# Kernel optimization log

Hardware: AMD Instinct MI355X
Metric: run time of the kernel (lower is better)

## Reference

```python
import jax, jax.numpy as jnp
import numpy as np

D_MODEL = 1024
N_HEADS = 16
HEAD_DIM = D_MODEL // N_HEADS
BATCH = 2
SEQ = 2048


def setup_inputs() -> dict:
    key = jax.random.key(0)
    ks = jax.random.split(key, 9)
    s = 1.0 / np.sqrt(D_MODEL)
    x = jax.random.normal(ks[0], (BATCH, SEQ, D_MODEL), dtype=jnp.float32)
    # causal mask, broadcastable to (B, H, S, S); positions with 0 are masked out
    mask = jnp.tril(jnp.ones((SEQ, SEQ), dtype=bool))[None, None, :, :]
    Wq = jax.random.normal(ks[1], (D_MODEL, D_MODEL), dtype=jnp.float32) * s
    Wk = jax.random.normal(ks[2], (D_MODEL, D_MODEL), dtype=jnp.float32) * s
    Wv = jax.random.normal(ks[3], (D_MODEL, D_MODEL), dtype=jnp.float32) * s
    Wo = jax.random.normal(ks[4], (D_MODEL, D_MODEL), dtype=jnp.float32) * s
    bq = jnp.zeros((D_MODEL,), jnp.float32)
    bk = jnp.zeros((D_MODEL,), jnp.float32)
    bv = jnp.zeros((D_MODEL,), jnp.float32)
    bo = jnp.zeros((D_MODEL,), jnp.float32)
    return {"x": x, "mask": mask, "Wq": Wq, "bq": bq, "Wk": Wk, "bk": bk,
            "Wv": Wv, "bv": bv, "Wo": Wo, "bo": bo}


def reference(x, mask, Wq, bq, Wk, bk, Wv, bv, Wo, bo):
    B, S, _ = x.shape
    scale = HEAD_DIM ** -0.5
    # nn.Linear: y = x @ W.T + b ; W stored as (out, in)
    def proj(W, b):
        y = jnp.einsum('bsd,ed->bse', x, W) + b
        return y.reshape(B, S, N_HEADS, HEAD_DIM).transpose(0, 2, 1, 3)  # (B,H,S,Dh)
    q = proj(Wq, bq)
    k = proj(Wk, bk)
    v = proj(Wv, bv)
    scores = jnp.einsum('bhqd,bhkd->bhqk', q, k) * scale  # (B,H,S,S)
    scores = jnp.where(mask, scores, jnp.float32(-jnp.inf))
    weights = jax.nn.softmax(scores, axis=-1)
    attn = jnp.einsum('bhqk,bhkd->bhqd', weights, v)
    attn = attn.transpose(0, 2, 1, 3).reshape(B, S, D_MODEL)
    out = jnp.einsum('bsd,ed->bse', attn, Wo) + bo
    return out
```

## Files before the change

kernel.cpp:

```cpp
#include <hip/hip_runtime.h>
#include <hip/hip_bf16.h>

using bf16x8 = __attribute__((ext_vector_type(8))) short;
using f32x4  = __attribute__((ext_vector_type(4))) float;

#define SEQ      2048
#define DMODEL   1024
#define NHEADS   16
#define HDIM     64
#define MROWS    4096

__device__ __forceinline__ unsigned short f2bf(float f) {
  union { float f; unsigned u; } c; c.f = f;
  unsigned r = c.u + 0x7FFFu + ((c.u >> 16) & 1u);
  return (unsigned short)(r >> 16);
}

__device__ __forceinline__ unsigned cvtpk(float a, float b) {
  unsigned r;
  asm("v_cvt_pk_bf16_f32 %0, %1, %2" : "=v"(r) : "v"(a), "v"(b));
  return r;
}

__device__ __forceinline__ void gload16(const void* g, void* s) {
  __builtin_amdgcn_global_load_lds(
      (const __attribute__((address_space(1))) void*)g,
      (__attribute__((address_space(3))) void*)s, 16, 0, 0);
}

__global__ void cvt_all(const float* __restrict__ x,  const float* __restrict__ wq,
                        const float* __restrict__ wk, const float* __restrict__ wv,
                        const float* __restrict__ wo,
                        unsigned short* __restrict__ xb,  unsigned short* __restrict__ wqb,
                        unsigned short* __restrict__ wkb, unsigned short* __restrict__ wvb,
                        unsigned short* __restrict__ wob)
{
  int i = blockIdx.x * blockDim.x + threadIdx.x;
  const float* src; unsigned short* dst; int off;
  if (i < 1048576) { src = x; dst = xb; off = i; }
  else {
    int k = i - 1048576, seg = k >> 18; off = k & 262143;
    if      (seg == 0) { src = wq; dst = wqb; }
    else if (seg == 1) { src = wk; dst = wkb; }
    else if (seg == 2) { src = wv; dst = wvb; }
    else               { src = wo; dst = wob; }
  }
  const float4 v = ((const float4*)src)[off];
  ushort4 o;
  o.x = f2bf(v.x); o.y = f2bf(v.y); o.z = f2bf(v.z); o.w = f2bf(v.w);
  ((ushort4*)dst)[off] = o;
}

__global__ __launch_bounds__(256, 4)
void gemm_qkv(const unsigned short* __restrict__ Ab,
              const unsigned short* __restrict__ Wqb,
              const unsigned short* __restrict__ Wkb,
              const unsigned short* __restrict__ Wvb,
              const float* __restrict__ bq, const float* __restrict__ bk,
              const float* __restrict__ bv,
              unsigned short* __restrict__ Qo, unsigned short* __restrict__ Ko,
              unsigned short* __restrict__ Vto)
{
  __shared__ unsigned short As[128 * 64];
  __shared__ unsigned short Bs[128 * 64];
  const int t  = threadIdx.x;
  const int w  = t >> 6, l = t & 63;
  const int lr = l & 15, lg = l >> 4;
  const int bm = blockIdx.x / 24;
  const int bn = blockIdx.x % 24;
  const int which = bn >> 3;
  const unsigned short* Bsrc = which == 0 ? Wqb : (which == 1 ? Wkb : Wvb);
  const float* biasp = which == 0 ? bq : (which == 1 ? bk : bv);
  const int bnw = bn & 7;
  const int wm = w >> 1, wn = w & 1;

  const char* Agp = (const char*)Ab + (size_t)bm * 128 * 2048;
  const char* Bgp = (const char*)Bsrc + (size_t)bnw * 128 * 2048;

  f32x4 acc[4][4];
  #pragma unroll
  for (int a = 0; a < 4; ++a)
    #pragma unroll
    for (int b = 0; b < 4; ++b) acc[a][b] = (f32x4){0.f, 0.f, 0.f, 0.f};

  for (int kt = 0; kt < 16; ++kt) {
    const int kbyte = kt * 128;
    #pragma unroll
    for (int i = 0; i < 4; ++i) {
      int idx  = i * 256 + t;
      int row  = idx >> 3;
      int colb = (idx & 7) << 4;
      gload16(Agp + (size_t)row * 2048 + kbyte + colb, (char*)As + idx * 16);
      gload16(Bgp + (size_t)row * 2048 + kbyte + colb, (char*)Bs + idx * 16);
    }
    __syncthreads();
    #pragma unroll
    for (int kk = 0; kk < 2; ++kk) {
      bf16x8 af[4], bfr[4];
      #pragma unroll
      for (int x = 0; x < 4; ++x) {
        af[x]  = *(const bf16x8*)&As[(wm * 64 + x * 16 + lr) * 64 + kk * 32 + lg * 8];
        bfr[x] = *(const bf16x8*)&Bs[(wn * 64 + x * 16 + lr) * 64 + kk * 32 + lg * 8];
      }
      #pragma unroll
      for (int xa = 0; xa < 4; ++xa)
        #pragma unroll
        for (int xb = 0; xb < 4; ++xb)
          acc[xa][xb] = __builtin_amdgcn_mfma_f32_16x16x32_bf16(af[xa], bfr[xb], acc[xa][xb], 0, 0, 0);
    }
    __syncthreads();
  }

  #pragma unroll
  for (int xb = 0; xb < 4; ++xb) {
    int colg = bnw * 128 + wn * 64 + xb * 16 + lr;
    int h  = colg >> 6, dh = colg & 63;
    float biasv = biasp[colg];
    #pragma unroll
    for (int xa = 0; xa < 4; ++xa) {
      int row0 = bm * 128 + wm * 64 + xa * 16 + lg * 4;
      #pragma unroll
      for (int i = 0; i < 4; ++i) {
        int m = row0 + i;
        int b = m >> 11, s = m & 2047;
        float v = acc[xa][xb][i] + biasv;
        if (which == 0) {
          Qo[(((size_t)(b * NHEADS + h)) * SEQ + s) * HDIM + dh] = f2bf(v * 0.180336881f);
        } else if (which == 1) {
          Ko[(((size_t)(b * NHEADS + h)) * SEQ + s) * HDIM + dh] = f2bf(v);
        } else {
          Vto[(((size_t)(b * NHEADS + h)) * HDIM + dh) * SEQ + s] = f2bf(v);
        }
      }
    }
  }
}

__device__ __forceinline__ void stage_kv64(const char* Kg, const char* Vg,
                                           char* Kl, char* Vl, int nb, int t)
{
  #pragma unroll
  for (int i = 0; i < 2; ++i) {
    int idx = i * 256 + t;
    int row = idx >> 3, colb = (idx & 7) << 4;
    int scol = colb ^ ((row & 7) << 4);
    gload16(Kg + (size_t)(nb + row) * 128 + scol, Kl + idx * 16);
    gload16(Vg + (size_t)row * 4096 + (size_t)nb * 2 + scol, Vl + idx * 16);
  }
}

__device__ __forceinline__ void attn_sub16(const char* Kl, const char* Vl, char* Pw,
                                           const bf16x8 (&qf)[2], const bf16x8 ones,
                                           f32x4 (&o)[4], f32x4 &accL,
                                           int q0w, int kbase, bool diag, int lr, int lg)
{
  bf16x8 kf[4][2];
  #pragma unroll
  for (int n = 0; n < 4; ++n)
    #pragma unroll
    for (int kk = 0; kk < 2; ++kk)
      kf[n][kk] = *(const bf16x8*)(Kl + (size_t)(n * 16 + lr) * 128 +
                                   ((kk * 64 + lg * 16) ^ ((lr & 7) << 4)));
  f32x4 st[4];
  __builtin_amdgcn_s_setprio(1);
  #pragma unroll
  for (int n = 0; n < 4; ++n) {
    f32x4 acc = (f32x4){0.f, 0.f, 0.f, 0.f};
    #pragma unroll
    for (int kk = 0; kk < 2; ++kk)
      acc = __builtin_amdgcn_mfma_f32_16x16x32_bf16(kf[n][kk], qf[kk], acc, 0, 0, 0);
    st[n] = acc;
  }
  __builtin_amdgcn_s_setprio(0);
  if (diag) {
    #pragma unroll
    for (int n = 0; n < 4; ++n) {
      #pragma unroll
      for (int i = 0; i < 4; ++i) {
        int key = kbase + n * 16 + lg * 4 + i;
        if (key > q0w + lr) st[n][i] = -3.0e38f;
      }
    }
  }
  #pragma unroll
  for (int n = 0; n < 4; ++n) {
    float p0 = exp2f(st[n][0]);
    float p1 = exp2f(st[n][1]);
    float p2 = exp2f(st[n][2]);
    float p3 = exp2f(st[n][3]);
    uint2 pw;
    pw.x = cvtpk(p0, p1);
    pw.y = cvtpk(p2, p3);
    *(uint2*)(Pw + lr * 128 + ((n * 32 + lg * 8) ^ ((lr & 7) << 4))) = pw;
  }
  __builtin_amdgcn_s_setprio(1);
  #pragma unroll
  for (int kk = 0; kk < 2; ++kk) {
    bf16x8 af = *(const bf16x8*)(Pw + lr * 128 + ((kk * 64 + lg * 16) ^ ((lr & 7) << 4)));
    accL = __builtin_amdgcn_mfma_f32_16x16x32_bf16(af, ones, accL, 0, 0, 0);
    #pragma unroll
    for (int n = 0; n < 4; ++n) {
      bf16x8 vf = *(const bf16x8*)(Vl + (size_t)(n * 16 + lr) * 128 +
                    ((kk * 64 + lg * 16) ^ ((lr & 7) << 4)));
      o[n] = __builtin_amdgcn_mfma_f32_16x16x32_bf16(af, vf, o[n], 0, 0, 0);
    }
  }
  __builtin_amdgcn_s_setprio(0);
}

__global__ __launch_bounds__(256, 4)
void attn_fwd(const unsigned short* __restrict__ Q,
              const unsigned short* __restrict__ K,
              const unsigned short* __restrict__ Vt,
              unsigned short* __restrict__ O)
{
  const int t = threadIdx.x;
  const int w = t >> 6, l = t & 63;
  const int lr = l & 15, lg = l >> 4;
  const int bh   = blockIdx.x & 31;
  const int slot = blockIdx.x >> 5;
  const int qt   = (slot < 8)  ? slot
                 : (slot < 16) ? (23 - slot)
                 : (slot < 24) ? slot
                 :               (55 - slot);
  const int b = bh >> 4, h = bh & 15;
  const int q0w = qt * 64 + w * 16;

  const unsigned short* Qp = Q + (size_t)bh * SEQ * HDIM;
  const char* Kg = (const char*)(K  + (size_t)bh * SEQ * HDIM);
  const char* Vg = (const char*)(Vt + (size_t)bh * HDIM * SEQ);

  __shared__ unsigned short Klds[2][64 * 64];
  __shared__ unsigned short Vlds[2][64 * 64];
  __shared__ unsigned short Plds[4][16][64];
  char* Pw = (char*)Plds[w];

  bf16x8 qf[2];
  #pragma unroll
  for (int kk = 0; kk < 2; ++kk)
    qf[kk] = *(const bf16x8*)(Qp + (size_t)(q0w + lr) * HDIM + kk * 32 + lg * 8);

  bf16x8 ones;
  #pragma unroll
  for (int e = 0; e < 8; ++e) ones[e] = (short)0x3F80;

  f32x4 o[4];
  f32x4 accL = (f32x4){0.f, 0.f, 0.f, 0.f};
  #pragma unroll
  for (int n = 0; n < 4; ++n) o[n] = (f32x4){0.f, 0.f, 0.f, 0.f};

  const int trips = qt + 1;

  stage_kv64(Kg, Vg, (char*)Klds[0], (char*)Vlds[0], 0, t);
  if (trips > 1)
    stage_kv64(Kg, Vg, (char*)Klds[1], (char*)Vlds[1], 64, t);

  int cur = 0;
  for (int kb = 0; kb < trips; ++kb) {
    if (kb + 1 < trips)
      asm volatile("s_waitcnt vmcnt(4)" ::: "memory");
    else
      asm volatile("s_waitcnt vmcnt(0)" ::: "memory");
    __builtin_amdgcn_s_barrier();
    asm volatile("" ::: "memory");
    attn_sub16((const char*)Klds[cur], (const char*)Vlds[cur], Pw, qf, ones,
               o, accL, q0w, kb * 64, kb == trips - 1, lr, lg);
    asm volatile("" ::: "memory");
    __builtin_amdgcn_s_barrier();
    asm volatile("" ::: "memory");
    if (kb + 2 < trips)
      stage_kv64(Kg, Vg, (char*)Klds[cur], (char*)Vlds[cur], (kb + 2) * 64, t);
    cur ^= 1;
  }

  #pragma unroll
  for (int n = 0; n < 4; ++n) {
    int col = h * HDIM + n * 16 + lr;
    #pragma unroll
    for (int i = 0; i < 4; ++i) {
      int srow = q0w + lg * 4 + i;
      O[((size_t)(b * SEQ + srow)) * DMODEL + col] = f2bf(o[n][i] / accL[i]);
    }
  }
}

__global__ __launch_bounds__(256, 2)
void gemm_out(const unsigned short* __restrict__ Ab, const unsigned short* __restrict__ Bb,
              const float* __restrict__ bias, float* __restrict__ C)
{
  __shared__ unsigned short As[128 * 64];
  __shared__ unsigned short Bs[64 * 64];
  const int t  = threadIdx.x;
  const int w  = t >> 6, l = t & 63;
  const int lr = l & 15, lg = l >> 4;
  const int bm = blockIdx.x >> 4;
  const int bn = blockIdx.x & 15;
  const int wm = w >> 1, wn = w & 1;

  const char* Agp = (const char*)Ab + (size_t)bm * 128 * 2048;
  const char* Bgp = (const char*)Bb + (size_t)bn * 64 * 2048;

  f32x4 acc[4][2];
  #pragma unroll
  for (int a = 0; a < 4; ++a)
    #pragma unroll
    for (int b = 0; b < 2; ++b) acc[a][b] = (f32x4){0.f, 0.f, 0.f, 0.f};

  for (int kt = 0; kt < 16; ++kt) {
    const int kbyte = kt * 128;
    #pragma unroll
    for (int i = 0; i < 4; ++i) {
      int idx  = i * 256 + t;
      int row  = idx >> 3;
      int colb = (idx & 7) << 4;
      gload16(Agp + (size_t)row * 2048 + kbyte + colb, (char*)As + idx * 16);
    }
    #pragma unroll
    for (int i = 0; i < 2; ++i) {
      int idx  = i * 256 + t;
      int row  = idx >> 3;
      int colb = (idx & 7) << 4;
      gload16(Bgp + (size_t)row * 2048 + kbyte + colb, (char*)Bs + idx * 16);
    }
    __syncthreads();
    #pragma unroll
    for (int kk = 0; kk < 2; ++kk) {
      bf16x8 af[4], bfr[2];
      #pragma unroll
      for (int x = 0; x < 4; ++x)
        af[x]  = *(const bf16x8*)&As[(wm * 64 + x * 16 + lr) * 64 + kk * 32 + lg * 8];
      #pragma unroll
      for (int x = 0; x < 2; ++x)
        bfr[x] = *(const bf16x8*)&Bs[(wn * 32 + x * 16 + lr) * 64 + kk * 32 + lg * 8];
      #pragma unroll
      for (int xa = 0; xa < 4; ++xa)
        #pragma unroll
        for (int xb = 0; xb < 2; ++xb)
          acc[xa][xb] = __builtin_amdgcn_mfma_f32_16x16x32_bf16(af[xa], bfr[xb], acc[xa][xb], 0, 0, 0);
    }
    __syncthreads();
  }
  #pragma unroll
  for (int xb = 0; xb < 2; ++xb) {
    int col = bn * 64 + wn * 32 + xb * 16 + lr;
    float bvv = bias[col];
    #pragma unroll
    for (int xa = 0; xa < 4; ++xa) {
      int row0 = bm * 128 + wm * 64 + xa * 16 + lg * 4;
      #pragma unroll
      for (int i = 0; i < 4; ++i)
        C[(size_t)(row0 + i) * DMODEL + col] = acc[xa][xb][i] + bvv;
    }
  }
}

extern "C" void kernel_launch(void* const* d_in, const int* in_sizes, int n_in,
                              void* d_out, int out_size, void* d_ws, size_t ws_size,
                              hipStream_t stream)
{
  const float* x  = (const float*)d_in[0];
  const float* Wq = (const float*)d_in[2];
  const float* bq = (const float*)d_in[3];
  const float* Wk = (const float*)d_in[4];
  const float* bk = (const float*)d_in[5];
  const float* Wv = (const float*)d_in[6];
  const float* bv = (const float*)d_in[7];
  const float* Wo = (const float*)d_in[8];
  const float* bo = (const float*)d_in[9];

  char* ws = (char*)d_ws;
  const size_t MB = 1024 * 1024;
  unsigned short* xb   = (unsigned short*)(ws + 0);
  unsigned short* Wqb  = (unsigned short*)(ws + 8  * MB);
  unsigned short* Wkb  = (unsigned short*)(ws + 10 * MB);
  unsigned short* Wvb  = (unsigned short*)(ws + 12 * MB);
  unsigned short* Wob  = (unsigned short*)(ws + 14 * MB);
  unsigned short* Qb   = (unsigned short*)(ws + 16 * MB);
  unsigned short* Kb   = (unsigned short*)(ws + 24 * MB);
  unsigned short* Vtb  = (unsigned short*)(ws + 32 * MB);
  unsigned short* Attn = (unsigned short*)(ws + 40 * MB);

  cvt_all<<<8192, 256, 0, stream>>>(x, Wq, Wk, Wv, Wo, xb, Wqb, Wkb, Wvb, Wob);
  gemm_qkv<<<768, 256, 0, stream>>>(xb, Wqb, Wkb, Wvb, bq, bk, bv, Qb, Kb, Vtb);
  attn_fwd<<<1024, 256, 0, stream>>>(Qb, Kb, Vtb, Attn);
  gemm_out<<<512, 256, 0, stream>>>(Attn, Wob, bo, (float*)d_out);
}
```

Baseline: 114.1 us.

## Pair causal q-tiles per block, swizzle GEMM LDS, use raw v_exp_f32

The attention kernel now gives each block two complementary query tiles (p and 31-p), so every block runs a uniform 33 KV iterations. This balances the causal triangle and halves the grid, with launch bounds lowered to 2 blocks per SU to make room for doubled accumulator registers. Both GEMMs gain an XOR swizzle on LDS columns to avoid bank conflicts on MFMA fragment reads. The softmax exp2f is replaced with raw v_exp_f32, which drops denormal and range handling. The costs are more registers per thread and lower occupancy in attention.

```diff
diff --git a/kernel.cpp b/kernel.cpp
--- a/kernel.cpp
+++ b/kernel.cpp
@@ -19,6 +19,12 @@
 __device__ __forceinline__ unsigned cvtpk(float a, float b) {
   unsigned r;
   asm("v_cvt_pk_bf16_f32 %0, %1, %2" : "=v"(r) : "v"(a), "v"(b));
+  return r;
+}
+
+__device__ __forceinline__ float fexp2(float x) {
+  float r;
+  asm("v_exp_f32 %0, %1" : "=v"(r) : "v"(x));
   return r;
 }
 
@@ -90,8 +96,9 @@
       int idx  = i * 256 + t;
       int row  = idx >> 3;
       int colb = (idx & 7) << 4;
-      gload16(Agp + (size_t)row * 2048 + kbyte + colb, (char*)As + idx * 16);
-      gload16(Bgp + (size_t)row * 2048 + kbyte + colb, (char*)Bs + idx * 16);
+      int scol = colb ^ ((row & 7) << 4);
+      gload16(Agp + (size_t)row * 2048 + kbyte + scol, (char*)As + idx * 16);
+      gload16(Bgp + (size_t)row * 2048 + kbyte + scol, (char*)Bs + idx * 16);
     }
     __syncthreads();
     #pragma unroll
@@ -99,8 +106,11 @@
       bf16x8 af[4], bfr[4];
       #pragma unroll
       for (int x = 0; x < 4; ++x) {
-        af[x]  = *(const bf16x8*)&As[(wm * 64 + x * 16 + lr) * 64 + kk * 32 + lg * 8];
-        bfr[x] = *(const bf16x8*)&Bs[(wn * 64 + x * 16 + lr) * 64 + kk * 32 + lg * 8];
+        int ra = wm * 64 + x * 16 + lr;
+        int rb = wn * 64 + x * 16 + lr;
+        int cb = (kk * 64 + lg * 16) ^ ((lr & 7) << 4);
+        af[x]  = *(const bf16x8*)((const char*)As + ra * 128 + cb);
+        bfr[x] = *(const bf16x8*)((const char*)Bs + rb * 128 + cb);
       }
       #pragma unroll
       for (int xa = 0; xa < 4; ++xa)
@@ -184,10 +194,10 @@
   }
   #pragma unroll
   for (int n = 0; n < 4; ++n) {
-    float p0 = exp2f(st[n][0]);
-    float p1 = exp2f(st[n][1]);
-    float p2 = exp2f(st[n][2]);
-    float p3 = exp2f(st[n][3]);
+    float p0 = fexp2(st[n][0]);
+    float p1 = fexp2(st[n][1]);
+    float p2 = fexp2(st[n][2]);
+    float p3 = fexp2(st[n][3]);
     uint2 pw;
     pw.x = cvtpk(p0, p1);
     pw.y = cvtpk(p2, p3);
@@ -208,7 +218,7 @@
   __builtin_amdgcn_s_setprio(0);
 }
 
-__global__ __launch_bounds__(256, 4)
+__global__ __launch_bounds__(256, 2)
 void attn_fwd(const unsigned short* __restrict__ Q,
               const unsigned short* __restrict__ K,
               const unsigned short* __restrict__ Vt,
@@ -217,14 +227,12 @@
   const int t = threadIdx.x;
   const int w = t >> 6, l = t & 63;
   const int lr = l & 15, lg = l >> 4;
-  const int bh   = blockIdx.x & 31;
-  const int slot = blockIdx.x >> 5;
-  const int qt   = (slot < 8)  ? slot
-                 : (slot < 16) ? (23 - slot)
-                 : (slot < 24) ? slot
-                 :               (55 - slot);
+  const int bh = blockIdx.x & 31;
+  const int p  = blockIdx.x >> 5;
+  const int qtA = p, qtB = 31 - p;
   const int b = bh >> 4, h = bh & 15;
-  const int q0w = qt * 64 + w * 16;
+  const int q0wA = qtA * 64 + w * 16;
+  const int q0wB = qtB * 64 + w * 16;
 
   const unsigned short* Qp = Q + (size_t)bh * SEQ * HDIM;
   const char* Kg = (const char*)(K  + (size_t)bh * SEQ * HDIM);
@@ -235,41 +243,56 @@
   __shared__ unsigned short Plds[4][16][64];
   char* Pw = (char*)Plds[w];
 
-  bf16x8 qf[2];
-  #pragma unroll
-  for (int kk = 0; kk < 2; ++kk)
-    qf[kk] = *(const bf16x8*)(Qp + (size_t)(q0w + lr) * HDIM + kk * 32 + lg * 8);
+  bf16x8 qfA[2], qfB[2];
+  #pragma unroll
+  for (int kk = 0; kk < 2; ++kk) {
+    qfA[kk] = *(const bf16x8*)(Qp + (size_t)(q0wA + lr) * HDIM + kk * 32 + lg * 8);
+    qfB[kk] = *(const bf16x8*)(Qp + (size_t)(q0wB + lr) * HDIM + kk * 32 + lg * 8);
+  }
 
   bf16x8 ones;
   #pragma unroll
   for (int e = 0; e < 8; ++e) ones[e] = (short)0x3F80;
 
-  f32x4 o[4];
-  f32x4 accL = (f32x4){0.f, 0.f, 0.f, 0.f};
-  #pragma unroll
-  for (int n = 0; n < 4; ++n) o[n] = (f32x4){0.f, 0.f, 0.f, 0.f};
-
-  const int trips = qt + 1;
+  f32x4 oA[4], oB[4];
+  f32x4 accLA = (f32x4){0.f, 0.f, 0.f, 0.f};
+  f32x4 accLB = (f32x4){0.f, 0.f, 0.f, 0.f};
+  #pragma unroll
+  for (int n = 0; n < 4; ++n) {
+    oA[n] = (f32x4){0.f, 0.f, 0.f, 0.f};
+    oB[n] = (f32x4){0.f, 0.f, 0.f, 0.f};
+  }
 
   stage_kv64(Kg, Vg, (char*)Klds[0], (char*)Vlds[0], 0, t);
-  if (trips > 1)
-    stage_kv64(Kg, Vg, (char*)Klds[1], (char*)Vlds[1], 64, t);
+  {
+    int kb1 = (1 <= qtA) ? 1 : 0;
+    stage_kv64(Kg, Vg, (char*)Klds[1], (char*)Vlds[1], kb1 * 64, t);
+  }
 
   int cur = 0;
-  for (int kb = 0; kb < trips; ++kb) {
-    if (kb + 1 < trips)
+  for (int j = 0; j < 33; ++j) {
+    if (j < 32)
       asm volatile("s_waitcnt vmcnt(4)" ::: "memory");
     else
       asm volatile("s_waitcnt vmcnt(0)" ::: "memory");
     __builtin_amdgcn_s_barrier();
     asm volatile("" ::: "memory");
-    attn_sub16((const char*)Klds[cur], (const char*)Vlds[cur], Pw, qf, ones,
-               o, accL, q0w, kb * 64, kb == trips - 1, lr, lg);
+    if (j <= qtA) {
+      attn_sub16((const char*)Klds[cur], (const char*)Vlds[cur], Pw, qfA, ones,
+                 oA, accLA, q0wA, j * 64, j == qtA, lr, lg);
+    } else {
+      int kb = j - qtA - 1;
+      attn_sub16((const char*)Klds[cur], (const char*)Vlds[cur], Pw, qfB, ones,
+                 oB, accLB, q0wB, kb * 64, j == 32, lr, lg);
+    }
     asm volatile("" ::: "memory");
     __builtin_amdgcn_s_barrier();
     asm volatile("" ::: "memory");
-    if (kb + 2 < trips)
-      stage_kv64(Kg, Vg, (char*)Klds[cur], (char*)Vlds[cur], (kb + 2) * 64, t);
+    if (j + 2 < 33) {
+      int jn = j + 2;
+      int kbn = (jn <= qtA) ? jn : jn - qtA - 1;
+      stage_kv64(Kg, Vg, (char*)Klds[cur], (char*)Vlds[cur], kbn * 64, t);
+    }
     cur ^= 1;
   }
 
@@ -278,8 +301,10 @@
     int col = h * HDIM + n * 16 + lr;
     #pragma unroll
     for (int i = 0; i < 4; ++i) {
-      int srow = q0w + lg * 4 + i;
-      O[((size_t)(b * SEQ + srow)) * DMODEL + col] = f2bf(o[n][i] / accL[i]);
+      int srowA = q0wA + lg * 4 + i;
+      int srowB = q0wB + lg * 4 + i;
+      O[((size_t)(b * SEQ + srowA)) * DMODEL + col] = f2bf(oA[n][i] / accLA[i]);
+      O[((size_t)(b * SEQ + srowB)) * DMODEL + col] = f2bf(oB[n][i] / accLB[i]);
     }
   }
 }
@@ -313,25 +338,33 @@
       int idx  = i * 256 + t;
       int row  = idx >> 3;
       int colb = (idx & 7) << 4;
-      gload16(Agp + (size_t)row * 2048 + kbyte + colb, (char*)As + idx * 16);
+      int scol = colb ^ ((row & 7) << 4);
+      gload16(Agp + (size_t)row * 2048 + kbyte + scol, (char*)As + idx * 16);
     }
     #pragma unroll
     for (int i = 0; i < 2; ++i) {
       int idx  = i * 256 + t;
       int row  = idx >> 3;
       int colb = (idx & 7) << 4;
-      gload16(Bgp + (size_t)row * 2048 + kbyte + colb, (char*)Bs + idx * 16);
+      int scol = colb ^ ((row & 7) << 4);
+      gload16(Bgp + (size_t)row * 2048 + kbyte + scol, (char*)Bs + idx * 16);
     }
     __syncthreads();
     #pragma unroll
     for (int kk = 0; kk < 2; ++kk) {
       bf16x8 af[4], bfr[2];
       #pragma unroll
-      for (int x = 0; x < 4; ++x)
-        af[x]  = *(const bf16x8*)&As[(wm * 64 + x * 16 + lr) * 64 + kk * 32 + lg * 8];
-      #pragma unroll
-      for (int x = 0; x < 2; ++x)
-        bfr[x] = *(const bf16x8*)&Bs[(wn * 32 + x * 16 + lr) * 64 + kk * 32 + lg * 8];
+      for (int x = 0; x < 4; ++x) {
+        int ra = wm * 64 + x * 16 + lr;
+        int cb = (kk * 64 + lg * 16) ^ ((lr & 7) << 4);
+        af[x]  = *(const bf16x8*)((const char*)As + ra * 128 + cb);
+      }
+      #pragma unroll
+      for (int x = 0; x < 2; ++x) {
+        int rb = wn * 32 + x * 16 + lr;
+        int cb = (kk * 64 + lg * 16) ^ ((lr & 7) << 4);
+        bfr[x] = *(const bf16x8*)((const char*)Bs + rb * 128 + cb);
+      }
       #pragma unroll
       for (int xa = 0; xa < 4; ++xa)
         #pragma unroll
@@ -382,6 +415,6 @@
 
   cvt_all<<<8192, 256, 0, stream>>>(x, Wq, Wk, Wv, Wo, xb, Wqb, Wkb, Wvb, Wob);
   gemm_qkv<<<768, 256, 0, stream>>>(xb, Wqb, Wkb, Wvb, bq, bk, bv, Qb, Kb, Vtb);
-  attn_fwd<<<1024, 256, 0, stream>>>(Qb, Kb, Vtb, Attn);
+  attn_fwd<<<512, 256, 0, stream>>>(Qb, Kb, Vtb, Attn);
   gemm_out<<<512, 256, 0, stream>>>(Attn, Wob, bo, (float*)d_out);
 }
```

After: 99.92 us. 12.4% less time.
